# Kernel tuning notes

Hardware: AMD Instinct MI355X
Metric: run time of the kernel (lower is better)

## Reference

```python
import jax, jax.numpy as jnp
import numpy as np

HEADS = 24
HEAD_DIM = 128
DIM = HEADS * HEAD_DIM  # 3072
EPS = 1e-6


def setup_inputs() -> dict:
    key = jax.random.key(0)
    ks = jax.random.split(key, 10)
    B, S_IMG, S_TXT = 1, 2048, 256
    hidden_states = jax.random.normal(ks[0], (B, S_IMG, DIM), jnp.float32)
    encoder_hidden_states = jax.random.normal(ks[1], (B, S_TXT, DIM), jnp.float32)
    # RoPE tables for image tokens, interleaved pair layout [S_IMG, HEAD_DIM]
    inv = 1.0 / (10000.0 ** (np.arange(0, HEAD_DIM, 2, dtype=np.float32) / HEAD_DIM))
    ang = np.arange(S_IMG, dtype=np.float32)[:, None] * inv[None, :]  # [S, Dh/2]
    ang = np.repeat(ang, 2, axis=-1)  # [S, Dh], pairs (2i, 2i+1) share angle
    rope_cos = jnp.asarray(np.cos(ang), jnp.float32)
    rope_sin = jnp.asarray(np.sin(ang), jnp.float32)
    s = 0.02
    wq = jax.random.normal(ks[2], (DIM, DIM), jnp.float32) * s
    wk = jax.random.normal(ks[3], (DIM, DIM), jnp.float32) * s
    wv = jax.random.normal(ks[4], (DIM, DIM), jnp.float32) * s
    wo = jax.random.normal(ks[5], (DIM, DIM), jnp.float32) * s
    bq = jax.random.normal(ks[6], (DIM,), jnp.float32) * s
    bk = jax.random.normal(ks[7], (DIM,), jnp.float32) * s
    bv = jax.random.normal(ks[8], (DIM,), jnp.float32) * s
    bo = jax.random.normal(ks[9], (DIM,), jnp.float32) * s
    norm_q_w = jnp.ones((HEAD_DIM,), jnp.float32)
    norm_k_w = jnp.ones((HEAD_DIM,), jnp.float32)
    return dict(hidden_states=hidden_states, encoder_hidden_states=encoder_hidden_states,
                rope_cos=rope_cos, rope_sin=rope_sin,
                wq=wq, bq=bq, wk=wk, bk=bk, wv=wv, bv=bv,
                norm_q_w=norm_q_w, norm_k_w=norm_k_w, wo=wo, bo=bo)


def _rmsnorm(x, w):
    var = jnp.mean(jnp.square(x), axis=-1, keepdims=True)
    return x * jax.lax.rsqrt(var + EPS) * w


def _rope(x, cos, sin):
    # x [B,H,S,Dh]; diffusers apply_rotary_emb with use_real_unbind_dim=-1:
    # pairs are interleaved (x[2i], x[2i+1]) -> rotated = stack(-imag, real)
    xr = x[..., 0::2]
    xi = x[..., 1::2]
    x_rot = jnp.stack([-xi, xr], axis=-1).reshape(x.shape)
    return x * cos + x_rot * sin


def reference(hidden_states, encoder_hidden_states, rope_cos, rope_sin,
              wq, bq, wk, bk, wv, bv, norm_q_w, norm_k_w, wo, bo):
    B, s_img, D = hidden_states.shape
    s_txt = encoder_hidden_states.shape[1]
    S = s_img + s_txt
    x = jnp.concatenate([hidden_states, encoder_hidden_states], axis=1)  # [B,S,D]

    def proj(w, b):
        return (x @ w + b).reshape(B, S, HEADS, HEAD_DIM).transpose(0, 2, 1, 3)  # [B,H,S,Dh]

    q = _rmsnorm(proj(wq, bq), norm_q_w)
    k = _rmsnorm(proj(wk, bk), norm_k_w)
    v = proj(wv, bv)
    # RoPE on image tokens only
    q = jnp.concatenate([_rope(q[:, :, :s_img], rope_cos, rope_sin), q[:, :, s_img:]], axis=2)
    k = jnp.concatenate([_rope(k[:, :, :s_img], rope_cos, rope_sin), k[:, :, s_img:]], axis=2)
    scale = 1.0 / jnp.sqrt(jnp.float32(HEAD_DIM))
    scores = jnp.einsum('bhqd,bhkd->bhqk', q, k) * scale
    attn = jax.nn.softmax(scores, axis=-1)
    out = jnp.einsum('bhqk,bhkd->bhqd', attn, v)
    out = out.transpose(0, 2, 1, 3).reshape(B, S, D)
    img = out[:, :s_img] @ wo + bo  # to_out[0]; to_out[1] is Dropout(p=0) -> identity
    txt = out[:, s_img:]            # to_add_out is None in this branch
    return img, txt
```

## Files before the change

kernel.cpp:

```cpp
#include <hip/hip_runtime.h>
#include <cstdint>

typedef __bf16 bf16_t;
typedef bf16_t bf16x8 __attribute__((ext_vector_type(8)));
typedef bf16_t bf16x4 __attribute__((ext_vector_type(4)));
typedef float  floatx4 __attribute__((ext_vector_type(4)));

#define S_ALL 2304
#define SIMG  2048
#define NH    24
#define HD    128
#define DIM   3072
#define NQKV  9216

#define SHIFT2 17.312340490667562f
#define QSCALE 0.12751744f

typedef __attribute__((address_space(1))) void* gp1_t;
typedef __attribute__((address_space(3))) void* lp3_t;

__device__ __forceinline__ void async16(const void* g, void* l) {
    __builtin_amdgcn_global_load_lds((gp1_t)(g), (lp3_t)(l), 16, 0, 0);
}
__device__ __forceinline__ floatx4 mfma_bf16(bf16x8 a, bf16x8 b, floatx4 c) {
    return __builtin_amdgcn_mfma_f32_16x16x32_bf16(a, b, c, 0, 0, 0);
}
__device__ __forceinline__ void barrier_raw() {
    asm volatile("s_barrier" ::: "memory");
}
template<int N> __device__ __forceinline__ void s_vmcnt() {
    if constexpr (N == 0)      asm volatile("s_waitcnt vmcnt(0)" ::: "memory");
    else if constexpr (N == 6) asm volatile("s_waitcnt vmcnt(6)" ::: "memory");
    else if constexpr (N == 8) asm volatile("s_waitcnt vmcnt(8)" ::: "memory");
}
template<int VH, int VL> __device__ __forceinline__ void vmcnt_w(int wave) {
    if constexpr (VH == VL) s_vmcnt<VH>();
    else { if (wave < 4) s_vmcnt<VH>(); else s_vmcnt<VL>(); }
}

__global__ __launch_bounds__(256) void k_convert_x(const float* __restrict__ hid,
                                                   const float* __restrict__ enc,
                                                   bf16_t* __restrict__ xb) {
    long i = ((long)blockIdx.x * 256 + threadIdx.x) * 4;
    const long HN = (long)SIMG * DIM;
    float4 f = (i < HN) ? *(const float4*)(hid + i) : *(const float4*)(enc + (i - HN));
    bf16x4 o;
    o[0] = (bf16_t)f.x; o[1] = (bf16_t)f.y; o[2] = (bf16_t)f.z; o[3] = (bf16_t)f.w;
    *(bf16x4*)(xb + i) = o;
}

__global__ __launch_bounds__(256) void k_wT4(const float* __restrict__ wq, const float* __restrict__ wk,
                                             const float* __restrict__ wv, const float* __restrict__ wo,
                                             bf16_t* __restrict__ wTq, bf16_t* __restrict__ woT) {
    __shared__ __align__(16) bf16_t T[64][72];
    int z = blockIdx.z;
    const float* W = (z == 0) ? wq : (z == 1) ? wk : (z == 2) ? wv : wo;
    bf16_t* Wt = (z < 3) ? (wTq + (long)z * DIM * DIM) : woT;
    int r0 = blockIdx.x * 64, c0 = blockIdx.y * 64;
    int tid = threadIdx.x;
    int lr = tid >> 2, lc = (tid & 3) * 16;
    const float* src = W + (long)(r0 + lr) * DIM + c0 + lc;
#pragma unroll
    for (int i = 0; i < 16; i += 4) {
        float4 f = *(const float4*)(src + i);
        T[lr][lc + i + 0] = (bf16_t)f.x;
        T[lr][lc + i + 1] = (bf16_t)f.y;
        T[lr][lc + i + 2] = (bf16_t)f.z;
        T[lr][lc + i + 3] = (bf16_t)f.w;
    }
    __syncthreads();
    bf16x8 a, b;
#pragma unroll
    for (int i = 0; i < 8; i++) a[i] = T[lc + i][lr];
#pragma unroll
    for (int i = 0; i < 8; i++) b[i] = T[lc + 8 + i][lr];
    bf16_t* dst = Wt + (long)(c0 + lr) * DIM + r0 + lc;
    *(bf16x8*)dst = a;
    *(bf16x8*)(dst + 8) = b;
}

template<int BM, int BN, int NWN, int AF, int VH, int VL>
__device__ __forceinline__ void gemm_pipe_s32(const bf16_t* __restrict__ A,
                                              const bf16_t* __restrict__ Bt,
                                              long m0, long n0, const int K,
                                              char* smem, int tid,
                                              floatx4 (&acc)[AF][4]) {
    constexpr int SLOTB = (BM + BN) * 64;
    constexpr int AH = AF / 2;
    const int wave = tid >> 6, lane = tid & 63;
    const int quad = lane >> 4, l16 = lane & 15;
    const int wm = (wave / NWN) * (AF * 16);
    const int wn = (wave % NWN) * 64;
    const int rsw = ((l16 >> 1) & 3) << 4;
    const int kc = ((lane & 3) ^ ((lane >> 3) & 3)) * 8;
    const bf16_t* Ag = A + (m0 + (lane >> 2)) * K + kc;
    const bf16_t* Bg = Bt + (n0 + (lane >> 2)) * K + kc;

    auto stageA = [&](int s) {
        char* base = smem + (s & 3) * SLOTB;
        const bf16_t* g = Ag + s * 32;
#pragma unroll
        for (int r0 = 0; r0 < BM; r0 += 128)
            if (BM - r0 >= 128 || wave * 16 < BM - r0)
                async16(g + (long)(r0 + wave * 16) * K, base + r0 * 64 + wave * 1024);
    };
    auto stageB = [&](int s) {
        char* base = smem + (s & 3) * SLOTB + BM * 64;
        const bf16_t* g = Bg + s * 32;
#pragma unroll
        for (int r0 = 0; r0 < BN; r0 += 128)
            if (BN - r0 >= 128 || wave * 16 < BN - r0)
                async16(g + (long)(r0 + wave * 16) * K, base + r0 * 64 + wave * 1024);
    };

    const int NS = K >> 5;

    stageA(0); stageB(0);
    stageA(1); stageB(1);
    stageA(2); stageB(2);
    vmcnt_w<VH, VL>(wave);
    barrier_raw();

    for (int s = 0; s < NS; ++s) {
        const char* sA = smem + (s & 3) * SLOTB;
        const char* sB = sA + BM * 64;
        const bool stg = (s < NS - 3);

        if (stg) stageA(s + 3);
        bf16x8 a0[AH], b0[4];
#pragma unroll
        for (int i = 0; i < AH; ++i)
            a0[i] = *(const bf16x8*)(sA + (wm + i * 16 + l16) * 64 + ((quad << 4) ^ rsw));
#pragma unroll
        for (int j = 0; j < 4; ++j)
            b0[j] = *(const bf16x8*)(sB + (wn + j * 16 + l16) * 64 + ((quad << 4) ^ rsw));
        barrier_raw();
        __builtin_amdgcn_s_setprio(1);
#pragma unroll
        for (int i = 0; i < AH; ++i)
#pragma unroll
            for (int j = 0; j < 4; ++j) acc[i][j] = mfma_bf16(a0[i], b0[j], acc[i][j]);
        __builtin_amdgcn_s_setprio(0);

        if (stg) stageB(s + 3);
        bf16x8 a1[AF - AH];
#pragma unroll
        for (int i = AH; i < AF; ++i)
            a1[i - AH] = *(const bf16x8*)(sA + (wm + i * 16 + l16) * 64 + ((quad << 4) ^ rsw));
        if (stg) vmcnt_w<VH, VL>(wave);
        else     s_vmcnt<0>();
        barrier_raw();
        __builtin_amdgcn_s_setprio(1);
#pragma unroll
        for (int i = AH; i < AF; ++i)
#pragma unroll
            for (int j = 0; j < 4; ++j) acc[i][j] = mfma_bf16(a1[i - AH], b0[j], acc[i][j]);
        __builtin_amdgcn_s_setprio(0);
    }
}

__global__ __launch_bounds__(512, 2) void k_gemm_qkv(const bf16_t* __restrict__ A,
                                                     const bf16_t* __restrict__ Bt,
                                                     const float* __restrict__ bq_,
                                                     const float* __restrict__ bk_,
                                                     const float* __restrict__ bv_,
                                                     const float* __restrict__ rope_cos,
                                                     const float* __restrict__ rope_sin,
                                                     const float* __restrict__ nqw,
                                                     const float* __restrict__ nkw,
                                                     bf16_t* __restrict__ qo,
                                                     bf16_t* __restrict__ ko,
                                                     bf16_t* __restrict__ vT) {
    __shared__ __align__(16) char smem[114688];
    int tid = threadIdx.x;
    int wave = tid >> 6, lane = tid & 63;
    int quad = lane >> 4, l16 = lane & 15;
    long m0 = (long)blockIdx.y * 192, n0 = (long)blockIdx.x * 256;
    int t = blockIdx.x / 12, hb = (blockIdx.x % 12) * 2;
    int wm = (wave >> 2) * 96;
    int h2w = (wave & 3) >> 1;
    int halfw = wave & 1;

    floatx4 zero = {0.f, 0.f, 0.f, 0.f};
    floatx4 acc[6][4];
#pragma unroll
    for (int i = 0; i < 6; i++)
#pragma unroll
        for (int j = 0; j < 4; j++) acc[i][j] = zero;

    gemm_pipe_s32<192, 256, 4, 6, 8, 6>(A, Bt, m0, n0, DIM, smem, tid, acc);

    int dcol[4];
#pragma unroll
    for (int j = 0; j < 4; j++) dcol[j] = halfw * 64 + j * 16 + l16;

    if (t == 2) {
        char* vbuf = smem;
#pragma unroll
        for (int h2 = 0; h2 < 2; ++h2) {
#pragma unroll
            for (int g3 = 0; g3 < 3; ++g3) {
                if (h2w == h2) {
                    float bias4[4];
#pragma unroll
                    for (int j = 0; j < 4; j++) bias4[j] = bv_[(hb + h2) * HD + dcol[j]];
#pragma unroll
                    for (int i = 0; i < 6; i++) {
                        if (((wm + i * 16) >> 6) == g3) {
#pragma unroll
                            for (int r = 0; r < 4; r++) {
                                int s_l = wm + i * 16 + quad * 4 + r - g3 * 64;
#pragma unroll
                                for (int j = 0; j < 4; j++) {
                                    int d = dcol[j];
                                    int chunk = d * 8 + ((s_l >> 3) ^ (d & 7));
                                    *(bf16_t*)(vbuf + chunk * 16 + (s_l & 7) * 2) =
                                        (bf16_t)(acc[i][j][r] + bias4[j]);
                                }
                            }
                        }
                    }
                }
                __syncthreads();
                int d = tid >> 2, sh = tid & 3;
                bf16_t* dstv = vT + (long)(hb + h2) * HD * S_ALL + (long)d * S_ALL
                             + m0 + g3 * 64;
#pragma unroll
                for (int u = 0; u < 2; ++u) {
                    int s8 = sh * 2 + u;
                    bf16x8 frag = *(const bf16x8*)(vbuf + (d * 8 + (s8 ^ (d & 7))) * 16);
                    *(bf16x8*)(dstv + s8 * 8) = frag;
                }
                __syncthreads();
            }
        }
    } else {
        float* ssq = (float*)smem;
        const float* bp = t ? bk_ : bq_;
        const float* nw = t ? nkw : nqw;
        int h = hb + h2w;
        float bias4[4], wv4[4];
#pragma unroll
        for (int j = 0; j < 4; j++) {
            bias4[j] = bp[h * HD + dcol[j]];
            wv4[j] = nw[dcol[j]];
        }
#pragma unroll
        for (int i = 0; i < 6; i++)
#pragma unroll
            for (int r = 0; r < 4; r++) {
                int row = wm + i * 16 + quad * 4 + r;
                float s2 = 0.f;
#pragma unroll
                for (int j = 0; j < 4; j++) {
                    float v = acc[i][j][r] + bias4[j];
                    acc[i][j][r] = v;
                    s2 += v * v;
                }
                s2 += __shfl_xor(s2, 1);
                s2 += __shfl_xor(s2, 2);
                s2 += __shfl_xor(s2, 4);
                s2 += __shfl_xor(s2, 8);
                if (l16 == 0) ssq[(h2w * 192 + row) * 2 + halfw] = s2;
            }
        __syncthreads();
        bf16_t* dst = (t ? ko : qo) + (long)h * S_ALL * HD;
#pragma unroll
        for (int i = 0; i < 6; i++)
#pragma unroll
            for (int r = 0; r < 4; r++) {
                int row = wm + i * 16 + quad * 4 + r;
                int s_abs = (int)m0 + row;
                float tot = ssq[(h2w * 192 + row) * 2] + ssq[(h2w * 192 + row) * 2 + 1];
                float rms = rsqrtf(tot * (1.0f / 128.0f) + 1e-6f);
                float y[4];
#pragma unroll
                for (int j = 0; j < 4; j++) y[j] = acc[i][j][r] * rms * wv4[j];
                if (s_abs < SIMG) {
                    const float* cp = rope_cos + (long)s_abs * HD;
                    const float* sp = rope_sin + (long)s_abs * HD;
#pragma unroll
                    for (int j = 0; j < 4; j++) {
                        float c = cp[dcol[j]], sn = sp[dcol[j]];
                        float px = __shfl_xor(y[j], 1);
                        y[j] = y[j] * c + ((l16 & 1) ? px : -px) * sn;
                    }
                }
#pragma unroll
                for (int j = 0; j < 4; j++) {
                    float v = t ? y[j] : y[j] * QSCALE;
                    dst[(long)s_abs * HD + dcol[j]] = (bf16_t)v;
                }
            }
    }
}

__global__ __launch_bounds__(512, 2) void k_gemm_bt(const bf16_t* __restrict__ A,
                                                    const bf16_t* __restrict__ Bt,
                                                    const float* __restrict__ bias,
                                                    bf16_t* __restrict__ Cb, float* __restrict__ Cf,
                                                    int M, int N, int K) {
    __shared__ __align__(16) char smem[98304];
    int tid = threadIdx.x;
    int wave = tid >> 6, lane = tid & 63;
    int quad = lane >> 4, l16 = lane & 15;
    long m0 = (long)blockIdx.y * 256, n0 = (long)blockIdx.x * 128;
    int wm = (wave >> 1) * 64, wn = (wave & 1) * 64;

    floatx4 zero = {0.f, 0.f, 0.f, 0.f};
    floatx4 acc[4][4];
#pragma unroll
    for (int i = 0; i < 4; i++)
#pragma unroll
        for (int j = 0; j < 4; j++) acc[i][j] = zero;

    gemm_pipe_s32<256, 128, 2, 4, 6, 6>(A, Bt, m0, n0, K, smem, tid, acc);

#pragma unroll
    for (int i = 0; i < 4; i++) {
        long rowb = m0 + wm + i * 16 + quad * 4;
#pragma unroll
        for (int j = 0; j < 4; j++) {
            long col = n0 + wn + j * 16 + l16;
            float bv = bias ? bias[col] : 0.0f;
#pragma unroll
            for (int r = 0; r < 4; r++) {
                float v = acc[i][j][r] + bv;
                long idx = (rowb + r) * N + col;
                if (Cb) Cb[idx] = (bf16_t)v;
                else    Cf[idx] = v;
            }
        }
    }
}

__global__ __launch_bounds__(256, 2) void k_attn(const bf16_t* __restrict__ q,
                                                 const bf16_t* __restrict__ k,
                                                 const bf16_t* __restrict__ vT,
                                                 bf16_t* __restrict__ ao,
                                                 float* __restrict__ out_txt) {
    __shared__ __align__(16) bf16_t Ks[64 * 128];
    __shared__ __align__(16) bf16_t VTs[128 * 64];
    __shared__ __align__(16) bf16_t Ps[4][2][16 * 64];
    int tid = threadIdx.x, wave = tid >> 6, lane = tid & 63;
    int quad = lane >> 4, l16 = lane & 15;
    int h = blockIdx.y;
    int q0 = blockIdx.x * 128 + wave * 32;
    const long hbase = (long)h * S_ALL * HD;
    const char* kgb = (const char*)(k + hbase);
    const char* vgb = (const char*)(vT + hbase);

    int koffB[4], voffB[4], slotB[4];
#pragma unroll
    for (int c2 = 0; c2 < 4; ++c2) {
        int L = (wave * 4 + c2) * 64 + lane;
        slotB[c2] = L;
        int rk = L >> 4, ck = (L & 15) ^ (rk & 15);
        koffB[c2] = rk * 256 + ck * 16;
        int rv = L >> 3, cv = (L & 7) ^ (rv & 7) ^ (((rv >> 3) & 1) << 2);
        voffB[c2] = rv * (S_ALL * 2) + cv * 16;
    }

    bf16x8 qf[2][4];
#pragma unroll
    for (int st = 0; st < 2; ++st) {
        const bf16_t* qp = q + hbase + (long)(q0 + st * 16 + l16) * HD + quad * 8;
#pragma unroll
        for (int ks = 0; ks < 4; ++ks) qf[st][ks] = *(const bf16x8*)(qp + ks * 32);
    }

    floatx4 zero = {0.f, 0.f, 0.f, 0.f};
    floatx4 o0[8], o1[8];
#pragma unroll
    for (int ni = 0; ni < 8; ++ni) { o0[ni] = zero; o1[ni] = zero; }
    floatx4 lac0 = zero, lac1 = zero;

    for (int kb = 0; kb < S_ALL / 64; ++kb) {
        const char* kg = kgb + (long)kb * 16384;
        const char* vg = vgb + kb * 128;
#pragma unroll
        for (int c2 = 0; c2 < 4; ++c2) {
            async16(kg + koffB[c2], (char*)Ks + slotB[c2] * 16);
            async16(vg + voffB[c2], (char*)VTs + slotB[c2] * 16);
        }
        __syncthreads();

        floatx4 s0[4], s1[4];
#pragma unroll
        for (int ni = 0; ni < 4; ++ni) { s0[ni] = zero; s1[ni] = zero; }
#pragma unroll
        for (int ks = 0; ks < 4; ++ks)
#pragma unroll
            for (int ni = 0; ni < 4; ++ni) {
                int slot = (ni * 16 + l16) * 16 + ((ks * 4 + quad) ^ l16);
                bf16x8 kf = *(const bf16x8*)&Ks[slot * 8];
                s0[ni] = mfma_bf16(qf[0][ks], kf, s0[ni]);
                s1[ni] = mfma_bf16(qf[1][ks], kf, s1[ni]);
            }

#pragma unroll
        for (int st = 0; st < 2; ++st) {
#pragma unroll
            for (int ni = 0; ni < 4; ++ni) {
                floatx4 sv = st ? s1[ni] : s0[ni];
                floatx4 p;
#pragma unroll
                for (int j = 0; j < 4; ++j) p[j] = __builtin_amdgcn_exp2f(sv[j] - SHIFT2);
                if (st) lac1 += p; else lac0 += p;
#pragma unroll
                for (int j = 0; j < 4; ++j) {
                    int r = quad * 4 + j;
                    int chunk = ((ni * 16 + l16) >> 3) ^ ((r >> 1) & 7);
                    Ps[wave][st][r * 64 + chunk * 8 + (l16 & 7)] = (bf16_t)p[j];
                }
            }
        }

        bf16x8 pf[2][2];
#pragma unroll
        for (int st = 0; st < 2; ++st)
#pragma unroll
            for (int k2 = 0; k2 < 2; ++k2) {
                int chunk = (k2 * 4 + quad) ^ ((l16 >> 1) & 7);
                pf[st][k2] = *(const bf16x8*)&Ps[wave][st][l16 * 64 + chunk * 8];
            }

#pragma unroll
        for (int k2 = 0; k2 < 2; ++k2)
#pragma unroll
            for (int ni = 0; ni < 8; ++ni) {
                int r = ni * 16 + l16;
                int c = (k2 * 4 + quad) ^ (l16 & 7) ^ (((l16 >> 3) & 1) << 2);
                bf16x8 vf = *(const bf16x8*)&VTs[r * 64 + c * 8];
                o0[ni] = mfma_bf16(pf[0][k2], vf, o0[ni]);
                o1[ni] = mfma_bf16(pf[1][k2], vf, o1[ni]);
            }
        __syncthreads();
    }

#pragma unroll
    for (int off = 1; off < 16; off <<= 1) {
#pragma unroll
        for (int j = 0; j < 4; ++j) {
            lac0[j] += __shfl_xor(lac0[j], off);
            lac1[j] += __shfl_xor(lac1[j], off);
        }
    }

#pragma unroll
    for (int st = 0; st < 2; ++st) {
#pragma unroll
        for (int j = 0; j < 4; ++j) {
            float rl = 1.0f / (st ? lac1[j] : lac0[j]);
            int s_row = q0 + st * 16 + quad * 4 + j;
#pragma unroll
            for (int ni = 0; ni < 8; ++ni) {
                float v = (st ? o1[ni][j] : o0[ni][j]) * rl;
                int col = h * HD + ni * 16 + l16;
                ao[(long)s_row * DIM + col] = (bf16_t)v;
                if (s_row >= SIMG) out_txt[(long)(s_row - SIMG) * DIM + col] = v;
            }
        }
    }
}

extern "C" void kernel_launch(void* const* d_in, const int* in_sizes, int n_in,
                              void* d_out, int out_size, void* d_ws, size_t ws_size,
                              hipStream_t stream) {
    const float* hid = (const float*)d_in[0];
    const float* enc = (const float*)d_in[1];
    const float* rope_cos = (const float*)d_in[2];
    const float* rope_sin = (const float*)d_in[3];
    const float* wq = (const float*)d_in[4];
    const float* bq = (const float*)d_in[5];
    const float* wk = (const float*)d_in[6];
    const float* bk = (const float*)d_in[7];
    const float* wv = (const float*)d_in[8];
    const float* bv = (const float*)d_in[9];
    const float* nqw = (const float*)d_in[10];
    const float* nkw = (const float*)d_in[11];
    const float* wo = (const float*)d_in[12];
    const float* bo = (const float*)d_in[13];
    float* out = (float*)d_out;

    char* ws = (char*)d_ws;
    bf16_t* xb   = (bf16_t*)(ws);
    bf16_t* wTq  = (bf16_t*)(ws + 14155776L);
    bf16_t* woT  = (bf16_t*)(ws + 70778880L);
    bf16_t* qb   = (bf16_t*)(ws + 89653248L);
    bf16_t* kbuf = (bf16_t*)(ws + 103809024L);
    bf16_t* vT   = (bf16_t*)(ws + 117964800L);
    bf16_t* ao   = (bf16_t*)(ws + 132120576L);

    k_convert_x<<<6912, 256, 0, stream>>>(hid, enc, xb);
    k_wT4<<<dim3(48, 48, 4), 256, 0, stream>>>(wq, wk, wv, wo, wTq, woT);
    k_gemm_qkv<<<dim3(36, 12), 512, 0, stream>>>(xb, wTq, bq, bk, bv, rope_cos, rope_sin,
                                                 nqw, nkw, qb, kbuf, vT);
    k_attn<<<dim3(18, 24), 256, 0, stream>>>(qb, kbuf, vT, ao, out + (long)SIMG * DIM);
    k_gemm_bt<<<dim3(24, 8), 512, 0, stream>>>(ao, woT, bo, (bf16_t*)nullptr, out, SIMG, DIM, DIM);
}
```

Measured before the change: 541.6 us.

## Enlarge QKV GEMM tile to 384x256 with per-head wave ownership

Rewrites the fused QKV projection kernel to use 384x256 block tiles, with each wave computing a 96x128 tile that covers a whole head. RMSNorm can then reduce within a wave via shuffles instead of through shared memory. The K loop becomes a 3-slot async-load pipeline with one barrier per step. The aim is more operand reuse and fewer epilogue barriers, at the cost of fewer blocks (216) and more registers and LDS per block.

New measurement: 611.1 us. +12.8%, slower.

```diff
diff --git a/kernel.cpp b/kernel.cpp
--- a/kernel.cpp
+++ b/kernel.cpp
@@ -30,6 +30,9 @@
 }
 template<int N> __device__ __forceinline__ void s_vmcnt() {
     if constexpr (N == 0)      asm volatile("s_waitcnt vmcnt(0)" ::: "memory");
+    else if constexpr (N == 2) asm volatile("s_waitcnt vmcnt(2)" ::: "memory");
+    else if constexpr (N == 3) asm volatile("s_waitcnt vmcnt(3)" ::: "memory");
+    else if constexpr (N == 5) asm volatile("s_waitcnt vmcnt(5)" ::: "memory");
     else if constexpr (N == 6) asm volatile("s_waitcnt vmcnt(6)" ::: "memory");
     else if constexpr (N == 8) asm volatile("s_waitcnt vmcnt(8)" ::: "memory");
 }
@@ -77,6 +80,177 @@
     bf16_t* dst = Wt + (long)(c0 + lr) * DIM + r0 + lc;
     *(bf16x8*)dst = a;
     *(bf16x8*)(dst + 8) = b;
+}
+
+__global__ __launch_bounds__(512, 2) void k_gemm_qkv(const bf16_t* __restrict__ A,
+                                                     const bf16_t* __restrict__ Bt,
+                                                     const float* __restrict__ bq_,
+                                                     const float* __restrict__ bk_,
+                                                     const float* __restrict__ bv_,
+                                                     const float* __restrict__ rope_cos,
+                                                     const float* __restrict__ rope_sin,
+                                                     const float* __restrict__ nqw,
+                                                     const float* __restrict__ nkw,
+                                                     bf16_t* __restrict__ qo,
+                                                     bf16_t* __restrict__ ko,
+                                                     bf16_t* __restrict__ vT) {
+    __shared__ __align__(16) char smem[122880];
+    constexpr int SLOTB = 40960;
+    const int K = DIM;
+    int tid = threadIdx.x;
+    int wave = tid >> 6, lane = tid & 63;
+    int quad = lane >> 4, l16 = lane & 15;
+    long m0 = (long)blockIdx.y * 384, n0 = (long)blockIdx.x * 256;
+    int t = blockIdx.x / 12, hb = (blockIdx.x % 12) * 2;
+    int wm = (wave >> 1) * 96;
+    int wnl = (wave & 1);
+    int wn = wnl * 128;
+
+    floatx4 zero = {0.f, 0.f, 0.f, 0.f};
+    floatx4 acc[6][8];
+#pragma unroll
+    for (int i = 0; i < 6; i++)
+#pragma unroll
+        for (int j = 0; j < 8; j++) acc[i][j] = zero;
+
+    {
+        const int rl = lane >> 2;
+        const int kb = ((lane & 3) ^ ((rl >> 1) & 3)) * 16;
+        const char* gb[5];
+#pragma unroll
+        for (int g = 0; g < 5; ++g) {
+            int cr = wave * 80 + g * 16 + rl;
+            gb[g] = (cr < 384) ? (const char*)(A + (m0 + cr) * K) + kb
+                               : (const char*)(Bt + (n0 + (cr - 384)) * K) + kb;
+        }
+        char* sbase0 = smem + wave * (80 * 64);
+
+        auto stage = [&](int s) {
+            char* base = sbase0 + (s % 3) * SLOTB;
+            const int kadv = s * 64;
+#pragma unroll
+            for (int g = 0; g < 5; ++g) async16(gb[g] + kadv, base + g * 1024);
+        };
+
+        const int NS = K >> 5;
+        stage(0); stage(1);
+        s_vmcnt<5>();
+        barrier_raw();
+
+        const int ch = ((quad ^ ((l16 >> 1) & 3)) << 4);
+        for (int s = 0; s < NS; ++s) {
+            const char* sA = smem + (s % 3) * SLOTB;
+            const char* sB = sA + 384 * 64;
+            const bool stg = (s + 2 < NS);
+            if (stg) stage(s + 2);
+
+            bf16x8 af[6], bf[8];
+#pragma unroll
+            for (int i = 0; i < 6; ++i)
+                af[i] = *(const bf16x8*)(sA + (wm + i * 16 + l16) * 64 + ch);
+#pragma unroll
+            for (int j = 0; j < 8; ++j)
+                bf[j] = *(const bf16x8*)(sB + (wn + j * 16 + l16) * 64 + ch);
+
+            __builtin_amdgcn_s_setprio(1);
+#pragma unroll
+            for (int i = 0; i < 6; ++i)
+#pragma unroll
+                for (int j = 0; j < 8; ++j) acc[i][j] = mfma_bf16(af[i], bf[j], acc[i][j]);
+            __builtin_amdgcn_s_setprio(0);
+
+            if (stg) s_vmcnt<5>();
+            else     s_vmcnt<0>();
+            barrier_raw();
+        }
+    }
+
+    int h = hb + wnl;
+    int dcol[8];
+#pragma unroll
+    for (int j = 0; j < 8; ++j) dcol[j] = j * 16 + l16;
+
+    if (t == 2) {
+        char* vbuf = smem;
+        float bias8[8];
+#pragma unroll
+        for (int j = 0; j < 8; ++j) bias8[j] = bv_[h * HD + dcol[j]];
+#pragma unroll
+        for (int hl = 0; hl < 2; ++hl) {
+            if (wnl == hl) {
+#pragma unroll
+                for (int i = 0; i < 6; ++i) {
+                    int s_l0 = wm + i * 16 + quad * 4;
+#pragma unroll
+                    for (int j = 0; j < 8; ++j) {
+                        int d = dcol[j];
+                        bf16x4 pk;
+#pragma unroll
+                        for (int r = 0; r < 4; ++r) pk[r] = (bf16_t)(acc[i][j][r] + bias8[j]);
+                        int chunk = d * 48 + ((s_l0 >> 3) ^ (d & 7));
+                        *(bf16x4*)(vbuf + chunk * 16 + (s_l0 & 7) * 2) = pk;
+                    }
+                }
+            }
+            __syncthreads();
+            int d = tid >> 2, sh = tid & 3;
+            bf16_t* dstv = vT + (long)(hb + hl) * HD * S_ALL + (long)d * S_ALL + m0;
+#pragma unroll
+            for (int u = 0; u < 12; ++u) {
+                int s8 = sh * 12 + u;
+                bf16x8 frag = *(const bf16x8*)(vbuf + (d * 48 + (s8 ^ (d & 7))) * 16);
+                *(bf16x8*)(dstv + s8 * 8) = frag;
+            }
+            __syncthreads();
+        }
+    } else {
+        const float* bp = t ? bk_ : bq_;
+        const float* nw = t ? nkw : nqw;
+        float bias8[8], wv8[8];
+#pragma unroll
+        for (int j = 0; j < 8; ++j) {
+            bias8[j] = bp[h * HD + dcol[j]];
+            wv8[j] = nw[dcol[j]];
+        }
+        bf16_t* dst = (t ? ko : qo) + (long)h * S_ALL * HD;
+#pragma unroll
+        for (int i = 0; i < 6; ++i)
+#pragma unroll
+            for (int r = 0; r < 4; ++r) {
+                int row = wm + i * 16 + quad * 4 + r;
+                int s_abs = (int)m0 + row;
+                float y[8];
+                float s2 = 0.f;
+#pragma unroll
+                for (int j = 0; j < 8; ++j) {
+                    float v = acc[i][j][r] + bias8[j];
+                    y[j] = v;
+                    s2 += v * v;
+                }
+                s2 += __shfl_xor(s2, 1);
+                s2 += __shfl_xor(s2, 2);
+                s2 += __shfl_xor(s2, 4);
+                s2 += __shfl_xor(s2, 8);
+                float rms = rsqrtf(s2 * (1.0f / 128.0f) + 1e-6f);
+#pragma unroll
+                for (int j = 0; j < 8; ++j) y[j] *= rms * wv8[j];
+                if (s_abs < SIMG) {
+                    const float* cp = rope_cos + (long)s_abs * HD;
+                    const float* sp = rope_sin + (long)s_abs * HD;
+#pragma unroll
+                    for (int j = 0; j < 8; ++j) {
+                        float c = cp[dcol[j]], sn = sp[dcol[j]];
+                        float px = __shfl_xor(y[j], 1);
+                        y[j] = y[j] * c + ((l16 & 1) ? px : -px) * sn;
+                    }
+                }
+#pragma unroll
+                for (int j = 0; j < 8; ++j) {
+                    float v = t ? y[j] : y[j] * QSCALE;
+                    dst[(long)s_abs * HD + dcol[j]] = (bf16_t)v;
+                }
+            }
+    }
 }
 
 template<int BM, int BN, int NWN, int AF, int VH, int VL>
@@ -156,142 +330,6 @@
 #pragma unroll
             for (int j = 0; j < 4; ++j) acc[i][j] = mfma_bf16(a1[i - AH], b0[j], acc[i][j]);
         __builtin_amdgcn_s_setprio(0);
-    }
-}
-
-__global__ __launch_bounds__(512, 2) void k_gemm_qkv(const bf16_t* __restrict__ A,
-                                                     const bf16_t* __restrict__ Bt,
-                                                     const float* __restrict__ bq_,
-                                                     const float* __restrict__ bk_,
-                                                     const float* __restrict__ bv_,
-                                                     const float* __restrict__ rope_cos,
-                                                     const float* __restrict__ rope_sin,
-                                                     const float* __restrict__ nqw,
-                                                     const float* __restrict__ nkw,
-                                                     bf16_t* __restrict__ qo,
-                                                     bf16_t* __restrict__ ko,
-                                                     bf16_t* __restrict__ vT) {
-    __shared__ __align__(16) char smem[114688];
-    int tid = threadIdx.x;
-    int wave = tid >> 6, lane = tid & 63;
-    int quad = lane >> 4, l16 = lane & 15;
-    long m0 = (long)blockIdx.y * 192, n0 = (long)blockIdx.x * 256;
-    int t = blockIdx.x / 12, hb = (blockIdx.x % 12) * 2;
-    int wm = (wave >> 2) * 96;
-    int h2w = (wave & 3) >> 1;
-    int halfw = wave & 1;
-
-    floatx4 zero = {0.f, 0.f, 0.f, 0.f};
-    floatx4 acc[6][4];
-#pragma unroll
-    for (int i = 0; i < 6; i++)
-#pragma unroll
-        for (int j = 0; j < 4; j++) acc[i][j] = zero;
-
-    gemm_pipe_s32<192, 256, 4, 6, 8, 6>(A, Bt, m0, n0, DIM, smem, tid, acc);
-
-    int dcol[4];
-#pragma unroll
-    for (int j = 0; j < 4; j++) dcol[j] = halfw * 64 + j * 16 + l16;
-
-    if (t == 2) {
-        char* vbuf = smem;
-#pragma unroll
-        for (int h2 = 0; h2 < 2; ++h2) {
-#pragma unroll
-            for (int g3 = 0; g3 < 3; ++g3) {
-                if (h2w == h2) {
-                    float bias4[4];
-#pragma unroll
-                    for (int j = 0; j < 4; j++) bias4[j] = bv_[(hb + h2) * HD + dcol[j]];
-#pragma unroll
-                    for (int i = 0; i < 6; i++) {
-                        if (((wm + i * 16) >> 6) == g3) {
-#pragma unroll
-                            for (int r = 0; r < 4; r++) {
-                                int s_l = wm + i * 16 + quad * 4 + r - g3 * 64;
-#pragma unroll
-                                for (int j = 0; j < 4; j++) {
-                                    int d = dcol[j];
-                                    int chunk = d * 8 + ((s_l >> 3) ^ (d & 7));
-                                    *(bf16_t*)(vbuf + chunk * 16 + (s_l & 7) * 2) =
-                                        (bf16_t)(acc[i][j][r] + bias4[j]);
-                                }
-                            }
-                        }
-                    }
-                }
-                __syncthreads();
-                int d = tid >> 2, sh = tid & 3;
-                bf16_t* dstv = vT + (long)(hb + h2) * HD * S_ALL + (long)d * S_ALL
-                             + m0 + g3 * 64;
-#pragma unroll
-                for (int u = 0; u < 2; ++u) {
-                    int s8 = sh * 2 + u;
-                    bf16x8 frag = *(const bf16x8*)(vbuf + (d * 8 + (s8 ^ (d & 7))) * 16);
-                    *(bf16x8*)(dstv + s8 * 8) = frag;
-                }
-                __syncthreads();
-            }
-        }
-    } else {
-        float* ssq = (float*)smem;
-        const float* bp = t ? bk_ : bq_;
-        const float* nw = t ? nkw : nqw;
-        int h = hb + h2w;
-        float bias4[4], wv4[4];
-#pragma unroll
-        for (int j = 0; j < 4; j++) {
-            bias4[j] = bp[h * HD + dcol[j]];
-            wv4[j] = nw[dcol[j]];
-        }
-#pragma unroll
-        for (int i = 0; i < 6; i++)
-#pragma unroll
-            for (int r = 0; r < 4; r++) {
-                int row = wm + i * 16 + quad * 4 + r;
-                float s2 = 0.f;
-#pragma unroll
-                for (int j = 0; j < 4; j++) {
-                    float v = acc[i][j][r] + bias4[j];
-                    acc[i][j][r] = v;
-                    s2 += v * v;
-                }
-                s2 += __shfl_xor(s2, 1);
-                s2 += __shfl_xor(s2, 2);
-                s2 += __shfl_xor(s2, 4);
-                s2 += __shfl_xor(s2, 8);
-                if (l16 == 0) ssq[(h2w * 192 + row) * 2 + halfw] = s2;
-            }
-        __syncthreads();
-        bf16_t* dst = (t ? ko : qo) + (long)h * S_ALL * HD;
-#pragma unroll
-        for (int i = 0; i < 6; i++)
-#pragma unroll
-            for (int r = 0; r < 4; r++) {
-                int row = wm + i * 16 + quad * 4 + r;
-                int s_abs = (int)m0 + row;
-                float tot = ssq[(h2w * 192 + row) * 2] + ssq[(h2w * 192 + row) * 2 + 1];
-                float rms = rsqrtf(tot * (1.0f / 128.0f) + 1e-6f);
-                float y[4];
-#pragma unroll
-                for (int j = 0; j < 4; j++) y[j] = acc[i][j][r] * rms * wv4[j];
-                if (s_abs < SIMG) {
-                    const float* cp = rope_cos + (long)s_abs * HD;
-                    const float* sp = rope_sin + (long)s_abs * HD;
-#pragma unroll
-                    for (int j = 0; j < 4; j++) {
-                        float c = cp[dcol[j]], sn = sp[dcol[j]];
-                        float px = __shfl_xor(y[j], 1);
-                        y[j] = y[j] * c + ((l16 & 1) ? px : -px) * sn;
-                    }
-                }
-#pragma unroll
-                for (int j = 0; j < 4; j++) {
-                    float v = t ? y[j] : y[j] * QSCALE;
-                    dst[(long)s_abs * HD + dcol[j]] = (bf16_t)v;
-                }
-            }
     }
 }
 
@@ -494,8 +532,8 @@
 
     k_convert_x<<<6912, 256, 0, stream>>>(hid, enc, xb);
     k_wT4<<<dim3(48, 48, 4), 256, 0, stream>>>(wq, wk, wv, wo, wTq, woT);
-    k_gemm_qkv<<<dim3(36, 12), 512, 0, stream>>>(xb, wTq, bq, bk, bv, rope_cos, rope_sin,
-                                                 nqw, nkw, qb, kbuf, vT);
+    k_gemm_qkv<<<dim3(36, 6), 512, 0, stream>>>(xb, wTq, bq, bk, bv, rope_cos, rope_sin,
+                                                nqw, nkw, qb, kbuf, vT);
     k_attn<<<dim3(18, 24), 256, 0, stream>>>(qb, kbuf, vT, ao, out + (long)SIMG * DIM);
     k_gemm_bt<<<dim3(24, 8), 512, 0, stream>>>(ao, woT, bo, (bf16_t*)nullptr, out, SIMG, DIM, DIM);
 }
```
